# Kernel optimization log

Hardware: AMD Instinct MI355X
Metric: run time of the kernel (lower is better)

The kernel has to match this reference:

```python
import jax, jax.numpy as jnp
import numpy as np

C = 1024
D = C // 8      # query/key channels
R = C // 16     # channel-attention reduction
B, H, W = 4, 64, 64


def setup_inputs() -> dict:
    key = jax.random.key(0)
    ks = jax.random.split(key, 10)
    s = lambda k, shp, fan: jax.random.normal(k, shp, jnp.float32) * (1.0 / np.sqrt(fan))
    return {
        "x": jax.random.normal(ks[0], (B, C, H, W), jnp.float32),
        "x1": jax.random.normal(ks[1], (B, C, H, W), jnp.float32),
        "Wq": s(ks[2], (D, C), C), "bq": jnp.zeros((D,), jnp.float32),
        "Wk": s(ks[3], (D, C), C), "bk": jnp.zeros((D,), jnp.float32),
        "Wv": s(ks[4], (C, C), C), "bv": jnp.zeros((C,), jnp.float32),
        "Wca1": s(ks[5], (R, C), C),  # CBAM MLP, no bias
        "Wca2": s(ks[6], (C, R), R),
    }


def _forward(x, x1, Wq, bq, Wk, bk, Wv, bv, Wca1, Wca2):
    b, c, h, w = x.shape
    n = h * w
    # 1x1 convs as channel matmuls
    Q = (jnp.einsum('bchw,dc->bdhw', x, Wq) + bq[:, None, None]).reshape(b, D, n)   # [B,D,N]
    K = (jnp.einsum('bchw,dc->bdhw', x, Wk) + bk[:, None, None]).reshape(b, D, n)   # [B,D,N]
    V = (jnp.einsum('bchw,oc->bohw', x1, Wv) + bv[:, None, None]).reshape(b, c, n)  # [B,C,N]
    # energy[b,n,m] = Q[:,n] . K[:,m]
    energy = jnp.einsum('bdn,bdm->bnm', Q, K)
    att = jax.nn.sigmoid(energy)                       # [B,N,N]
    # torch: bmm(V, att^T) -> out[b,c,n] = sum_m V[b,c,m] * att[b,n,m]
    out = jnp.einsum('bcm,bnm->bcn', V, att).reshape(b, c, h, w)
    # ChannelAttention (CBAM): shared MLP on avg+max pooled features, sigmoid gate
    avg = out.mean(axis=(2, 3))                        # [B,C]
    mx = out.max(axis=(2, 3))                          # [B,C]
    mlp = lambda v: jnp.einsum('cr,br->bc', Wca2, jax.nn.relu(jnp.einsum('rc,bc->br', Wca1, v)))
    gate = jax.nn.sigmoid(mlp(avg) + mlp(mx))          # [B,C]
    return out * gate[:, :, None, None]


def reference(x, x1, Wq, bq, Wk, bk, Wv, bv, Wca1, Wca2):
    return _forward(x, x1, Wq, bq, Wk, bk, Wv, bv, Wca1, Wca2)
```

## Files before the change

### kernel.cpp

```cpp
#include <hip/hip_runtime.h>
#include <hip/hip_fp16.h>
#include <cstdint>

typedef _Float16 f16;
typedef __attribute__((ext_vector_type(8))) _Float16 half8;
typedef __attribute__((ext_vector_type(16))) float floatx16;

#define CC 1024
#define DD 128
#define RRR 64
#define BBATCH 4
#define NNN 4096

#define BM 128
#define BN 128
#define BK 64

__device__ __forceinline__ void gl_lds16(const void* g, void* l) {
  __builtin_amdgcn_global_load_lds(
      (__attribute__((address_space(1))) void*)(uintptr_t)g,
      (__attribute__((address_space(3))) void*)l, 16, 0, 0);
}

template<int EPI>
__global__ __launch_bounds__(256)
void gemm_bt(const f16* __restrict__ A, const f16* __restrict__ Bp, f16* __restrict__ Cout,
             const float* __restrict__ bias, int N, int K,
             int lda, int ldb, int ldc, size_t sA, size_t sB, size_t sC)
{
  __shared__ __align__(16) f16 S[2 * BM * BK];
  f16* As = S;
  f16* Bs = S + BM * BK;

  const int z = blockIdx.z;
  const int tid  = threadIdx.x;
  const int lane = tid & 63;
  const int wave = tid >> 6;
  const int m0 = blockIdx.y * BM;
  const int n0 = blockIdx.x * BN;
  const int wm = (wave >> 1) * 64;
  const int wn = (wave & 1) * 64;
  const int l31 = lane & 31;
  const int hi  = lane >> 5;
  const int rs  = lane & 7;

  const f16* Ab = A  + (size_t)z * sA + (size_t)m0 * lda;
  const f16* Bb = Bp + (size_t)z * sB + (size_t)n0 * ldb;

  floatx16 acc[2][2];
#pragma unroll
  for (int i = 0; i < 2; ++i)
#pragma unroll
    for (int j = 0; j < 2; ++j)
#pragma unroll
      for (int r = 0; r < 16; ++r)
        acc[i][j][r] = 0.f;

  int srow[4], ssrc[4];
#pragma unroll
  for (int r = 0; r < 4; ++r) {
    const int gi = r * 256 + tid;
    const int row = gi >> 3;
    const int gc  = gi & 7;
    srow[r] = row;
    ssrc[r] = ((gc ^ (row & 7)) << 3);
  }

  for (int k0 = 0; k0 < K; k0 += BK) {
#pragma unroll
    for (int r = 0; r < 4; ++r) {
      gl_lds16(Ab + (size_t)srow[r] * lda + k0 + ssrc[r], As + (size_t)(r * 256 + tid) * 8);
      gl_lds16(Bb + (size_t)srow[r] * ldb + k0 + ssrc[r], Bs + (size_t)(r * 256 + tid) * 8);
    }
    __syncthreads();

#pragma unroll
    for (int kk = 0; kk < BK; kk += 16) {
      const int gr = (((kk >> 3) + hi) ^ rs) << 3;
      half8 af[2], bfr[2];
#pragma unroll
      for (int i = 0; i < 2; ++i)
        af[i] = *(const half8*)(As + (wm + i * 32 + l31) * BK + gr);
#pragma unroll
      for (int j = 0; j < 2; ++j)
        bfr[j] = *(const half8*)(Bs + (wn + j * 32 + l31) * BK + gr);
#pragma unroll
      for (int i = 0; i < 2; ++i)
#pragma unroll
        for (int j = 0; j < 2; ++j)
          acc[i][j] = __builtin_amdgcn_mfma_f32_32x32x16_f16(af[i], bfr[j], acc[i][j], 0, 0, 0);
    }
    __syncthreads();
  }

  f16* Ch = Cout + (size_t)z * sC;
  f16* Ct = S;
#pragma unroll
  for (int i = 0; i < 2; ++i)
#pragma unroll
    for (int j = 0; j < 2; ++j)
#pragma unroll
      for (int r = 0; r < 16; ++r) {
        const int rl = wm + i * 32 + (r & 3) + 8 * (r >> 2) + 4 * hi;
        const int cl = wn + j * 32 + l31;
        const float v = acc[i][j][r];
        f16 h;
        if constexpr (EPI == 0)      h = (f16)v;
        else if constexpr (EPI == 1) h = (f16)(v + bias[m0 + rl]);
        else if constexpr (EPI == 2) h = (f16)(v + bias[n0 + cl]);
        else                         h = (f16)(1.0f / (1.0f + __expf(-v)));
        Ct[rl * BN + ((((cl >> 3) ^ (rl & 7)) << 3) | (cl & 7))] = h;
      }
  __syncthreads();
#pragma unroll
  for (int p = 0; p < 8; ++p) {
    const int idx = p * 256 + tid;
    const int rl = idx >> 4;
    const int g  = idx & 15;
    half8 vv = *(const half8*)(Ct + rl * BN + ((g ^ (rl & 7)) << 3));
    *(half8*)(Ch + (size_t)(m0 + rl) * ldc + n0 + g * 8) = vv;
  }
}

__global__ __launch_bounds__(256)
void prep(const float* __restrict__ Wq, const float* __restrict__ Wk, const float* __restrict__ Wv,
          const float* __restrict__ bq, const float* __restrict__ bk,
          f16* __restrict__ WQKb, f16* __restrict__ Wvb, float* __restrict__ bqk)
{
  const int NV = CC * CC;
  const int NQ = DD * CC;
  int i = blockIdx.x * 256 + threadIdx.x;
  if (i < NV)                    Wvb[i] = (f16)Wv[i];
  else if (i < NV + NQ)          WQKb[i - NV] = (f16)Wq[i - NV];
  else if (i < NV + 2 * NQ)      WQKb[i - NV] = (f16)Wk[i - NV - NQ];
  else if (i < NV + 2 * NQ + 2 * DD) {
    int t = i - NV - 2 * NQ;
    bqk[t] = (t < DD) ? bq[t] : bk[t - DD];
  }
}

__global__ __launch_bounds__(256)
void transpose_cvt(const float* __restrict__ x, const float* __restrict__ x1,
                   f16* __restrict__ ox, f16* __restrict__ ox1, int nb)
{
  const int zz = blockIdx.z;
  const int b  = (zz < nb) ? zz : zz - nb;
  const float* in = ((zz < nb) ? x : x1) + (size_t)b * CC * NNN;
  f16* out = ((zz < nb) ? ox : ox1) + (size_t)b * CC * NNN;
  __shared__ float tile[32][33];
  const int c0 = blockIdx.y * 32;
  const int n0 = blockIdx.x * 32;
  const int tx = threadIdx.x & 31;
  const int ty = threadIdx.x >> 5;
#pragma unroll
  for (int r = 0; r < 32; r += 8)
    tile[ty + r][tx] = in[(size_t)(c0 + ty + r) * NNN + n0 + tx];
  __syncthreads();
#pragma unroll
  for (int r = 0; r < 32; r += 8)
    out[(size_t)(n0 + ty + r) * CC + c0 + tx] = (f16)tile[tx][ty + r];
}

__global__ __launch_bounds__(256)
void rowreduce(const f16* __restrict__ X, float* __restrict__ avg, float* __restrict__ mx, int ncols)
{
  const size_t ridx = (size_t)blockIdx.y * gridDim.x + blockIdx.x;
  const half8* p = (const half8*)(X + ridx * ncols);
  float s = 0.f, m = -3.402823466e38f;
  for (int i = threadIdx.x; i < ncols / 8; i += 256) {
    half8 v = p[i];
#pragma unroll
    for (int e = 0; e < 8; ++e) {
      float f = (float)v[e];
      s += f;
      m = fmaxf(m, f);
    }
  }
#pragma unroll
  for (int o = 32; o > 0; o >>= 1) {
    s += __shfl_down(s, o);
    m = fmaxf(m, __shfl_down(m, o));
  }
  __shared__ float ss[4], sm[4];
  if ((threadIdx.x & 63) == 0) { ss[threadIdx.x >> 6] = s; sm[threadIdx.x >> 6] = m; }
  __syncthreads();
  if (threadIdx.x == 0) {
    s = ss[0] + ss[1] + ss[2] + ss[3];
    m = fmaxf(fmaxf(sm[0], sm[1]), fmaxf(sm[2], sm[3]));
    avg[ridx] = s / (float)ncols;
    mx[ridx] = m;
  }
}

__global__ __launch_bounds__(256)
void mlp_gate(const float* __restrict__ avg, const float* __restrict__ mxv,
              const float* __restrict__ W1, const float* __restrict__ W2,
              float* __restrict__ gate)
{
  const int z = blockIdx.x;
  avg += (size_t)z * CC; mxv += (size_t)z * CC; gate += (size_t)z * CC;
  const int t = threadIdx.x;
  const int r = t & 63;
  const int part = t >> 6;
  __shared__ float pa[4][64], pm[4][64], h[RRR];
  {
    const float* w = W1 + (size_t)r * CC + part * 256;
    const float* av = avg + part * 256;
    const float* mv = mxv + part * 256;
    float sa = 0.f, sm = 0.f;
    for (int c = 0; c < 256; ++c) { float wv = w[c]; sa += wv * av[c]; sm += wv * mv[c]; }
    pa[part][r] = sa; pm[part][r] = sm;
  }
  __syncthreads();
  if (t < RRR) {
    float A_ = pa[0][t] + pa[1][t] + pa[2][t] + pa[3][t];
    float M_ = pm[0][t] + pm[1][t] + pm[2][t] + pm[3][t];
    h[t] = fmaxf(A_, 0.f) + fmaxf(M_, 0.f);
  }
  __syncthreads();
  for (int c = t; c < CC; c += 256) {
    float s = 0.f;
    for (int rr = 0; rr < RRR; ++rr) s += W2[(size_t)c * RRR + rr] * h[rr];
    gate[c] = 1.0f / (1.0f + __expf(-s));
  }
}

__global__ __launch_bounds__(256)
void scale_out(const f16* __restrict__ oh, float* __restrict__ out, const float* __restrict__ gate)
{
  oh  += (size_t)blockIdx.y * CC * NNN;
  out += (size_t)blockIdx.y * CC * NNN;
  gate += (size_t)blockIdx.y * CC;
  size_t i = (size_t)blockIdx.x * 256 + threadIdx.x;
  half8 v = ((const half8*)oh)[i];
  const float g = gate[(i * 8) >> 12];
  float4 a = { (float)v[0] * g, (float)v[1] * g, (float)v[2] * g, (float)v[3] * g };
  float4 b = { (float)v[4] * g, (float)v[5] * g, (float)v[6] * g, (float)v[7] * g };
  float4* o = (float4*)out;
  o[2 * i]     = a;
  o[2 * i + 1] = b;
}

extern "C" void kernel_launch(void* const* d_in, const int* in_sizes, int n_in,
                              void* d_out, int out_size, void* d_ws, size_t ws_size,
                              hipStream_t stream)
{
  const float* x    = (const float*)d_in[0];
  const float* x1   = (const float*)d_in[1];
  const float* Wq   = (const float*)d_in[2];
  const float* bq   = (const float*)d_in[3];
  const float* Wk   = (const float*)d_in[4];
  const float* bk   = (const float*)d_in[5];
  const float* Wv   = (const float*)d_in[6];
  const float* bv   = (const float*)d_in[7];
  const float* Wca1 = (const float*)d_in[8];
  const float* Wca2 = (const float*)d_in[9];
  float* out = (float*)d_out;

  char* ws = (char*)d_ws;
  size_t off = 0;
  auto alloc = [&](size_t bytes) { void* p = ws + off; off += (bytes + 255) & ~255ULL; return p; };

  f16* WQKb = (f16*)alloc((size_t)2 * DD * CC * 2);
  f16* Wvb  = (f16*)alloc((size_t)CC * CC * 2);
  float* bqk  = (float*)alloc(256 * 4);
  float* avg  = (float*)alloc((size_t)BBATCH * CC * 4);
  float* mxv  = (float*)alloc((size_t)BBATCH * CC * 4);
  float* gate = (float*)alloc((size_t)BBATCH * CC * 4);

  const size_t attB = (size_t)NNN * NNN * 2;
  const size_t xTB  = (size_t)BBATCH * NNN * CC * 2;
  const size_t qkB  = (size_t)BBATCH * NNN * 2 * DD * 2;
  const size_t vBB  = (size_t)BBATCH * CC * NNN * 2;
  const size_t ohB  = (size_t)BBATCH * CC * NNN * 2;
  const size_t fixedEnd = off;

  int g = 0;
  for (int cand = BBATCH; cand >= 1; cand >>= 1) {
    size_t need = fixedEnd + 2 * xTB + qkB + vBB + ohB + (size_t)cand * attB + (1 << 20);
    if (need <= ws_size) { g = cand; break; }
  }

  const dim3 blk(256);
  const int prepN = CC * CC + 2 * DD * CC + 2 * DD;
  prep<<<(prepN + 255) / 256, blk, 0, stream>>>(Wq, Wk, Wv, bq, bk, WQKb, Wvb, bqk);

  if (g > 0) {
    f16* xTb  = (f16*)alloc(xTB);
    f16* x1Tb = (f16*)alloc(xTB);
    f16* QKt  = (f16*)alloc(qkB);
    f16* Vb   = (f16*)alloc(vBB);
    f16* outh = (f16*)alloc(ohB);
    f16* att  = (f16*)alloc((size_t)g * attB);

    transpose_cvt<<<dim3(NNN / 32, CC / 32, 2 * BBATCH), blk, 0, stream>>>(x, x1, xTb, x1Tb, BBATCH);

    gemm_bt<2><<<dim3(2 * DD / BN, NNN / BM, BBATCH), blk, 0, stream>>>(
        xTb, WQKb, QKt, bqk, 2 * DD, CC,
        CC, CC, 2 * DD, (size_t)NNN * CC, 0, (size_t)NNN * 2 * DD);
    gemm_bt<1><<<dim3(NNN / BN, CC / BM, BBATCH), blk, 0, stream>>>(
        Wvb, x1Tb, Vb, bv, NNN, CC,
        CC, CC, NNN, 0, (size_t)NNN * CC, (size_t)CC * NNN);

    for (int b0 = 0; b0 < BBATCH; b0 += g) {
      const int gc = (b0 + g <= BBATCH) ? g : (BBATCH - b0);
      const size_t sQK = (size_t)NNN * 2 * DD;
      gemm_bt<3><<<dim3(NNN / BN, NNN / BM, gc), blk, 0, stream>>>(
          QKt + (size_t)b0 * sQK, QKt + (size_t)b0 * sQK + DD, att, nullptr,
          NNN, DD, 2 * DD, 2 * DD, NNN, sQK, sQK, (size_t)NNN * NNN);
      gemm_bt<0><<<dim3(NNN / BN, CC / BM, gc), blk, 0, stream>>>(
          Vb + (size_t)b0 * CC * NNN, att, outh + (size_t)b0 * CC * NNN, nullptr,
          NNN, NNN, NNN, NNN, NNN,
          (size_t)CC * NNN, (size_t)NNN * NNN, (size_t)CC * NNN);
    }

    rowreduce<<<dim3(CC, BBATCH), blk, 0, stream>>>(outh, avg, mxv, NNN);
    mlp_gate<<<BBATCH, blk, 0, stream>>>(avg, mxv, Wca1, Wca2, gate);
    scale_out<<<dim3(CC * NNN / 8 / 256, BBATCH), blk, 0, stream>>>(outh, out, gate);
  } else {
    f16* xTb  = (f16*)alloc((size_t)NNN * CC * 2);
    f16* x1Tb = (f16*)alloc((size_t)NNN * CC * 2);
    f16* QKt  = (f16*)alloc((size_t)NNN * 2 * DD * 2);
    f16* Vb   = (f16*)alloc((size_t)CC * NNN * 2);
    f16* outh = (f16*)alloc((size_t)CC * NNN * 2);
    f16* att  = (f16*)alloc(attB);

    for (int b = 0; b < BBATCH; ++b) {
      const float* xb  = x  + (size_t)b * CC * NNN;
      const float* x1b = x1 + (size_t)b * CC * NNN;
      float* outb = out + (size_t)b * CC * NNN;

      transpose_cvt<<<dim3(NNN / 32, CC / 32, 2), blk, 0, stream>>>(xb, x1b, xTb, x1Tb, 1);

      gemm_bt<2><<<dim3(2 * DD / BN, NNN / BM, 1), blk, 0, stream>>>(
          xTb, WQKb, QKt, bqk, 2 * DD, CC, CC, CC, 2 * DD, 0, 0, 0);
      gemm_bt<1><<<dim3(NNN / BN, CC / BM, 1), blk, 0, stream>>>(
          Wvb, x1Tb, Vb, bv, NNN, CC, CC, CC, NNN, 0, 0, 0);
      gemm_bt<3><<<dim3(NNN / BN, NNN / BM, 1), blk, 0, stream>>>(
          QKt, QKt + DD, att, nullptr, NNN, DD, 2 * DD, 2 * DD, NNN, 0, 0, 0);
      gemm_bt<0><<<dim3(NNN / BN, CC / BM, 1), blk, 0, stream>>>(
          Vb, att, outh, nullptr, NNN, NNN, NNN, NNN, NNN, 0, 0, 0);

      rowreduce<<<dim3(CC, 1), blk, 0, stream>>>(outh, avg + (size_t)b * CC, mxv + (size_t)b * CC, NNN);
      mlp_gate<<<1, blk, 0, stream>>>(avg + (size_t)b * CC, mxv + (size_t)b * CC, Wca1, Wca2, gate + (size_t)b * CC);
      scale_out<<<dim3(CC * NNN / 8 / 256, 1), blk, 0, stream>>>(outh, outb, gate + (size_t)b * CC);
    }
  }
}
```

Baseline: 530.5 us.

## Add 256x256 8-wave MFMA GEMM for V and output; alias transposes into attention buffer

Result: faster. 483.7 us (-8.8%).

```diff
diff --git a/kernel.cpp b/kernel.cpp
--- a/kernel.cpp
+++ b/kernel.cpp
@@ -122,6 +122,153 @@
   }
 }
 
+#define G8_STAGE(MATG, MIDX, LD, H, KT, BUF) do {                                   \
+    gl_lds16(MATG + (size_t)((H) * 128 + srow) * (LD) + (KT) * 64 + soff,           \
+             &S[BUF][MIDX][(H) * 8192 + tid * 8]);                                  \
+    gl_lds16(MATG + (size_t)((H) * 128 + 64 + srow) * (LD) + (KT) * 64 + soff,      \
+             &S[BUF][MIDX][(H) * 8192 + 4096 + tid * 8]);                           \
+  } while (0)
+
+#define G8_LOADA(QM) do {                                                           \
+    _Pragma("unroll") for (int mt = 0; mt < 2; ++mt)                                \
+    _Pragma("unroll") for (int ks = 0; ks < 4; ++ks)                                \
+      af[mt * 4 + ks] = *(const half8*)(Ac + aRow + ((QM) * 2 + mt) * 2048 + sws[ks]); \
+  } while (0)
+
+#define G8_LOADB(NT2) do {                                                          \
+    _Pragma("unroll") for (int ks = 0; ks < 4; ++ks)                                \
+      bf[(NT2) * 4 + ks] = *(const half8*)(Bc + bRow + (NT2) * 2048 + sws[ks]);     \
+  } while (0)
+
+#define G8_MFMA(QM, QN) do {                                                        \
+    __builtin_amdgcn_s_setprio(1);                                                  \
+    _Pragma("unroll") for (int mt = 0; mt < 2; ++mt)                                \
+    _Pragma("unroll") for (int ks = 0; ks < 4; ++ks)                                \
+      acc[(QM) * 2 + mt][QN] = __builtin_amdgcn_mfma_f32_32x32x16_f16(              \
+          af[mt * 4 + ks], bf[(QN) * 4 + ks], acc[(QM) * 2 + mt][QN], 0, 0, 0);     \
+    __builtin_amdgcn_s_setprio(0);                                                  \
+  } while (0)
+
+template<int EPI>
+__global__ __launch_bounds__(512, 2)
+void gemm8p(const f16* __restrict__ A, const f16* __restrict__ Bp, f16* __restrict__ Cout,
+            const float* __restrict__ bias, int K,
+            int lda, int ldb, int ldc, size_t sA, size_t sB, size_t sC)
+{
+  __shared__ __align__(16) f16 S[2][2][16384];
+
+  const int tid  = threadIdx.x;
+  const int lane = tid & 63;
+  const int wave = tid >> 6;
+  const int wm   = wave >> 2;
+  const int wn   = wave & 3;
+  const int l31  = lane & 31;
+  const int hi   = lane >> 5;
+  const int z    = blockIdx.z;
+  const int m0   = blockIdx.y * 256;
+  const int n0   = blockIdx.x * 256;
+
+  const f16* Ag = A  + (size_t)z * sA + (size_t)m0 * lda;
+  const f16* Bg = Bp + (size_t)z * sB + (size_t)n0 * ldb;
+
+  const int srow = tid >> 3;
+  const int soff = (((tid & 7) ^ (srow & 7)) << 3);
+
+  int sws[4];
+#pragma unroll
+  for (int ks = 0; ks < 4; ++ks) sws[ks] = (((ks * 2 + hi) ^ (l31 & 7)) << 3);
+  const int aRow = (wm * 128 + l31) * 64;
+  const int bRow = (wn * 64 + l31) * 64;
+
+  floatx16 acc[4][2];
+#pragma unroll
+  for (int i = 0; i < 4; ++i)
+#pragma unroll
+    for (int j = 0; j < 2; ++j)
+#pragma unroll
+      for (int r = 0; r < 16; ++r) acc[i][j][r] = 0.f;
+
+  half8 af[8], bf[8];
+
+  G8_STAGE(Ag, 0, lda, 0, 0, 0);
+  G8_STAGE(Bg, 1, ldb, 0, 0, 0);
+  G8_STAGE(Ag, 0, lda, 1, 0, 0);
+  G8_STAGE(Bg, 1, ldb, 1, 0, 0);
+
+  const int NT = K >> 6;
+  for (int t = 0; t < NT; ++t) {
+    const int cur = t & 1, nxt = cur ^ 1;
+    const f16* Ac = &S[cur][0][0];
+    const f16* Bc = &S[cur][1][0];
+    const bool pf = (t + 1 < NT);
+
+    if (pf) {
+      G8_STAGE(Ag, 0, lda, 0, t + 1, nxt);
+      G8_STAGE(Bg, 1, ldb, 0, t + 1, nxt);
+      asm volatile("s_waitcnt vmcnt(4)" ::: "memory");
+    } else {
+      asm volatile("s_waitcnt vmcnt(0)" ::: "memory");
+    }
+    __builtin_amdgcn_s_barrier();
+    G8_LOADA(0); G8_LOADB(0);
+    asm volatile("s_waitcnt lgkmcnt(0)" ::: "memory");
+    __builtin_amdgcn_sched_barrier(0);
+    G8_MFMA(0, 0);
+    __builtin_amdgcn_s_barrier();
+
+    G8_LOADB(1);
+    if (pf) G8_STAGE(Ag, 0, lda, 1, t + 1, nxt);
+    __builtin_amdgcn_s_barrier();
+    asm volatile("s_waitcnt lgkmcnt(0)" ::: "memory");
+    __builtin_amdgcn_sched_barrier(0);
+    G8_MFMA(0, 1);
+    __builtin_amdgcn_s_barrier();
+
+    G8_LOADA(1);
+    if (pf) G8_STAGE(Bg, 1, ldb, 1, t + 1, nxt);
+    __builtin_amdgcn_s_barrier();
+    asm volatile("s_waitcnt lgkmcnt(0)" ::: "memory");
+    __builtin_amdgcn_sched_barrier(0);
+    G8_MFMA(1, 1);
+    __builtin_amdgcn_s_barrier();
+
+    G8_MFMA(1, 0);
+    __builtin_amdgcn_s_barrier();
+  }
+
+  f16* Ct = &S[0][0][0];
+  f16* Ch = Cout + (size_t)z * sC;
+#pragma unroll
+  for (int i = 0; i < 4; ++i)
+#pragma unroll
+    for (int j = 0; j < 2; ++j)
+#pragma unroll
+      for (int r = 0; r < 16; ++r) {
+        const int rl = wm * 128 + i * 32 + (r & 3) + 8 * (r >> 2) + 4 * hi;
+        const int cl = wn * 64 + j * 32 + l31;
+        const float v = acc[i][j][r];
+        f16 h;
+        if constexpr (EPI == 1) h = (f16)(v + bias[m0 + rl]);
+        else                    h = (f16)v;
+        Ct[rl * 256 + ((((cl >> 3) ^ (rl & 7)) << 3) | (cl & 7))] = h;
+      }
+  asm volatile("s_waitcnt lgkmcnt(0)" ::: "memory");
+  __builtin_amdgcn_s_barrier();
+#pragma unroll
+  for (int p = 0; p < 16; ++p) {
+    const int idx = p * 512 + tid;
+    const int rl = idx >> 5;
+    const int g  = idx & 31;
+    half8 vv = *(const half8*)(Ct + rl * 256 + ((g ^ (rl & 7)) << 3));
+    *(half8*)(Ch + (size_t)(m0 + rl) * ldc + n0 + g * 8) = vv;
+  }
+}
+
+#undef G8_STAGE
+#undef G8_LOADA
+#undef G8_LOADB
+#undef G8_MFMA
+
 __global__ __launch_bounds__(256)
 void prep(const float* __restrict__ Wq, const float* __restrict__ Wk, const float* __restrict__ Wv,
           const float* __restrict__ bq, const float* __restrict__ bk,
@@ -147,18 +294,30 @@
   const int b  = (zz < nb) ? zz : zz - nb;
   const float* in = ((zz < nb) ? x : x1) + (size_t)b * CC * NNN;
   f16* out = ((zz < nb) ? ox : ox1) + (size_t)b * CC * NNN;
-  __shared__ float tile[32][33];
-  const int c0 = blockIdx.y * 32;
-  const int n0 = blockIdx.x * 32;
-  const int tx = threadIdx.x & 31;
-  const int ty = threadIdx.x >> 5;
-#pragma unroll
-  for (int r = 0; r < 32; r += 8)
-    tile[ty + r][tx] = in[(size_t)(c0 + ty + r) * NNN + n0 + tx];
+  __shared__ float tile[64][65];
+  const int c0 = blockIdx.y * 64;
+  const int n0 = blockIdx.x * 64;
+  const int t  = threadIdx.x;
+  const int rn = (t & 15) * 4;
+  const int rc = t >> 4;
+#pragma unroll
+  for (int r = 0; r < 4; ++r) {
+    const float4 v = *(const float4*)(in + (size_t)(c0 + rc + r * 16) * NNN + n0 + rn);
+    tile[rc + r * 16][rn]     = v.x;
+    tile[rc + r * 16][rn + 1] = v.y;
+    tile[rc + r * 16][rn + 2] = v.z;
+    tile[rc + r * 16][rn + 3] = v.w;
+  }
   __syncthreads();
-#pragma unroll
-  for (int r = 0; r < 32; r += 8)
-    out[(size_t)(n0 + ty + r) * CC + c0 + tx] = (f16)tile[tx][ty + r];
+  const int ce = (t & 7) * 8;
+  const int nr = t >> 3;
+#pragma unroll
+  for (int r = 0; r < 2; ++r) {
+    half8 vv;
+#pragma unroll
+    for (int e = 0; e < 8; ++e) vv[e] = (f16)tile[ce + e][nr + r * 32];
+    *(half8*)(out + (size_t)(n0 + nr + r * 32) * CC + c0 + ce) = vv;
+  }
 }
 
 __global__ __launch_bounds__(256)
@@ -275,15 +434,50 @@
   const size_t ohB  = (size_t)BBATCH * CC * NNN * 2;
   const size_t fixedEnd = off;
 
+  const dim3 blk(256);
+  const int prepN = CC * CC + 2 * DD * CC + 2 * DD;
+  prep<<<(prepN + 255) / 256, blk, 0, stream>>>(Wq, Wk, Wv, bq, bk, WQKb, Wvb, bqk);
+
+  {
+    size_t offF = fixedEnd;
+    auto af_ = [&](size_t bytes) { void* p = ws + offF; offF += (bytes + 255) & ~255ULL; return p; };
+    f16* QKt  = (f16*)af_(qkB);
+    f16* Vb   = (f16*)af_(vBB);
+    f16* outh = (f16*)af_(ohB);
+    f16* att  = (f16*)af_((size_t)BBATCH * attB);
+    if (offF + (1 << 20) <= ws_size) {
+      f16* xTb  = att;
+      f16* x1Tb = att + (size_t)BBATCH * NNN * CC;
+
+      transpose_cvt<<<dim3(NNN / 64, CC / 64, 2 * BBATCH), blk, 0, stream>>>(x, x1, xTb, x1Tb, BBATCH);
+
+      gemm_bt<2><<<dim3(2 * DD / BN, NNN / BM, BBATCH), blk, 0, stream>>>(
+          xTb, WQKb, QKt, bqk, 2 * DD, CC,
+          CC, CC, 2 * DD, (size_t)NNN * CC, 0, (size_t)NNN * 2 * DD);
+      gemm8p<1><<<dim3(NNN / 256, CC / 256, BBATCH), dim3(512), 0, stream>>>(
+          Wvb, x1Tb, Vb, bv, CC,
+          CC, CC, NNN, 0, (size_t)NNN * CC, (size_t)CC * NNN);
+
+      const size_t sQK = (size_t)NNN * 2 * DD;
+      gemm_bt<3><<<dim3(NNN / BN, NNN / BM, BBATCH), blk, 0, stream>>>(
+          QKt, QKt + DD, att, nullptr, NNN, DD,
+          2 * DD, 2 * DD, NNN, sQK, sQK, (size_t)NNN * NNN);
+      gemm8p<0><<<dim3(NNN / 256, CC / 256, BBATCH), dim3(512), 0, stream>>>(
+          Vb, att, outh, nullptr, NNN,
+          NNN, NNN, NNN, (size_t)CC * NNN, (size_t)NNN * NNN, (size_t)CC * NNN);
+
+      rowreduce<<<dim3(CC, BBATCH), blk, 0, stream>>>(outh, avg, mxv, NNN);
+      mlp_gate<<<BBATCH, blk, 0, stream>>>(avg, mxv, Wca1, Wca2, gate);
+      scale_out<<<dim3(CC * NNN / 8 / 256, BBATCH), blk, 0, stream>>>(outh, out, gate);
+      return;
+    }
+  }
+
   int g = 0;
   for (int cand = BBATCH; cand >= 1; cand >>= 1) {
     size_t need = fixedEnd + 2 * xTB + qkB + vBB + ohB + (size_t)cand * attB + (1 << 20);
     if (need <= ws_size) { g = cand; break; }
   }
-
-  const dim3 blk(256);
-  const int prepN = CC * CC + 2 * DD * CC + 2 * DD;
-  prep<<<(prepN + 255) / 256, blk, 0, stream>>>(Wq, Wk, Wv, bq, bk, WQKb, Wvb, bqk);
 
   if (g > 0) {
     f16* xTb  = (f16*)alloc(xTB);
@@ -293,7 +487,7 @@
     f16* outh = (f16*)alloc(ohB);
     f16* att  = (f16*)alloc((size_t)g * attB);
 
-    transpose_cvt<<<dim3(NNN / 32, CC / 32, 2 * BBATCH), blk, 0, stream>>>(x, x1, xTb, x1Tb, BBATCH);
+    transpose_cvt<<<dim3(NNN / 64, CC / 64, 2 * BBATCH), blk, 0, stream>>>(x, x1, xTb, x1Tb, BBATCH);
 
     gemm_bt<2><<<dim3(2 * DD / BN, NNN / BM, BBATCH), blk, 0, stream>>>(
         xTb, WQKb, QKt, bqk, 2 * DD, CC,
@@ -330,7 +524,7 @@
       const float* x1b = x1 + (size_t)b * CC * NNN;
       float* outb = out + (size_t)b * CC * NNN;
 
-      transpose_cvt<<<dim3(NNN / 32, CC / 32, 2), blk, 0, stream>>>(xb, x1b, xTb, x1Tb, 1);
+      transpose_cvt<<<dim3(NNN / 64, CC / 64, 2), blk, 0, stream>>>(xb, x1b, xTb, x1Tb, 1);
 
       gemm_bt<2><<<dim3(2 * DD / BN, NNN / BM, 1), blk, 0, stream>>>(
           xTb, WQKb, QKt, bqk, 2 * DD, CC, CC, CC, 2 * DD, 0, 0, 0);
```
